# Kernel optimization log

Hardware: AMD Instinct MI355X
Metric: run time of the kernel (lower is better)

Reference implementation:

```python
import jax, jax.numpy as jnp
import numpy as np

N_NODES = 100000
N_EDGES = 1600000
N_GRAPHS = 256
D = 128
L = 3
N_OUT = 10


def setup_inputs() -> dict:
    key = jax.random.key(0)
    ks = jax.random.split(key, 6)
    x = jax.random.normal(ks[0], (N_NODES, D), dtype=jnp.float32)
    edge_index = jax.random.randint(ks[1], (2, N_EDGES), 0, N_NODES, dtype=jnp.int64)
    batch = jnp.sort(jax.random.randint(ks[2], (N_NODES,), 0, N_GRAPHS, dtype=jnp.int64))
    conv_w = jax.random.normal(ks[3], (L, D, D), dtype=jnp.float32) * (1.0 / np.sqrt(D))
    conv_b = jnp.zeros((L, D), dtype=jnp.float32)
    out_w = jax.random.normal(ks[4], (3 * D, N_OUT), dtype=jnp.float32) * (1.0 / np.sqrt(3 * D))
    out_b = jnp.zeros((N_OUT,), dtype=jnp.float32)
    return {"x": x, "edge_index": edge_index, "batch": batch,
            "conv_w": conv_w, "conv_b": conv_b, "out_w": out_w, "out_b": out_b}


def reference(x, edge_index, batch, conv_w, conv_b, out_w, out_b):
    N = x.shape[0]
    # --- add self-loops (PyG GCNConv default) ---
    loop = jnp.arange(N, dtype=edge_index.dtype)
    src = jnp.concatenate([edge_index[0], loop])  # [E+N]
    dst = jnp.concatenate([edge_index[1], loop])
    # --- symmetric normalization: deg computed on dst (col) ---
    deg = jax.ops.segment_sum(jnp.ones_like(dst, dtype=x.dtype), dst, num_segments=N)
    dinv = jnp.where(deg > 0, jax.lax.rsqrt(jnp.maximum(deg, 1.0)), 0.0)
    norm = dinv[src] * dinv[dst]  # [E+N]

    h = x
    for l in range(conv_w.shape[0]):
        h = h @ conv_w[l]                                   # [N, D] transform first
        msg = h[src] * norm[:, None]                        # gather + scale
        h = jax.ops.segment_sum(msg, dst, num_segments=N)   # scatter-add
        h = jax.nn.relu(h + conv_b[l])

    # --- global max / mean / add pooling over graphs ---
    B = N_GRAPHS
    gmax = jax.ops.segment_max(h, batch, num_segments=B)
    gsum = jax.ops.segment_sum(h, batch, num_segments=B)
    cnt = jax.ops.segment_sum(jnp.ones((N, 1), h.dtype), batch, num_segments=B)
    gmean = gsum / jnp.maximum(cnt, 1.0)
    pooled = jnp.concatenate([gmax, gmean, gsum], axis=1)   # [B, 3D]
    # dropout p=0.5 is identity in eval mode
    return pooled @ out_w + out_b
```

## Files before the change

kernel.cpp:

```cpp
#include <hip/hip_runtime.h>
#include <hip/hip_bf16.h>

#define D 128
#define NP 8
#define DPB 64
#define KPB (DPB * NP)
#define SUB 64
#define CAP_SUB 64

typedef __attribute__((ext_vector_type(8))) __bf16 bf16x8;
typedef __attribute__((ext_vector_type(4))) float f32x4;
typedef __attribute__((ext_vector_type(4))) short s16x4;
typedef __attribute__((ext_vector_type(8))) short s16x8;

static __device__ __forceinline__ short f2bf(float f) {
    union { float f; unsigned u; } in; in.f = f;
    unsigned u = in.u;
    u += 0x7fffu + ((u >> 16) & 1u);
    return (short)(u >> 16);
}

__global__ void k_bucket(const int* __restrict__ src, const int* __restrict__ dst,
                         int* __restrict__ bcnt, int* __restrict__ staging,
                         int E, int KBE) {
    int i = blockIdx.x * 256 + threadIdx.x;
    if (i >= E) return;
    int d = dst[i], s = src[i];
    int b = d >> 6;
    int key = ((d & 63) << 3) | (s >> 14);
    int j = blockIdx.x & (SUB - 1);
    int slot = atomicAdd(&bcnt[j * KBE + b], 1);
    if (slot < CAP_SUB) staging[((size_t)j * KBE + b) * CAP_SUB + slot] = (key << 17) | s;
}

__global__ void k_btot(const int* __restrict__ bcnt, int* __restrict__ btot, int KBE) {
    int b = blockIdx.x * 256 + threadIdx.x;
    if (b >= KBE) return;
    int v = 0;
    #pragma unroll
    for (int j = 0; j < SUB; j++) {
        int c = bcnt[j * KBE + b];
        v += (c > CAP_SUB) ? CAP_SUB : c;
    }
    btot[b] = v;
}

__global__ void k_bscan(const int* __restrict__ btot, int* __restrict__ bbase,
                        int* __restrict__ row_ptr, int nkeys, int KBE) {
    __shared__ int sm[512];
    __shared__ int carry;
    int t = threadIdx.x;
    if (t == 0) carry = 0;
    __syncthreads();
    for (int c0 = 0; c0 < KBE; c0 += 512) {
        int b = c0 + t;
        int v = (b < KBE) ? btot[b] : 0;
        sm[t] = v;
        __syncthreads();
        for (int off = 1; off < 512; off <<= 1) {
            int x = (t >= off) ? sm[t - off] : 0;
            __syncthreads();
            sm[t] += x;
            __syncthreads();
        }
        if (b < KBE) bbase[b] = sm[t] - v + carry;
        __syncthreads();
        if (t == 0) carry += sm[511];
        __syncthreads();
    }
    if (t == 0) { bbase[KBE] = carry; row_ptr[nkeys] = carry; }
}

__global__ __launch_bounds__(256) void k_build(
    const int* __restrict__ staging, const int* __restrict__ bcnt,
    const int* __restrict__ bbase, int* __restrict__ row_ptr,
    int* __restrict__ csr_src, float* __restrict__ dinv, int N, int KBE)
{
    const int b = blockIdx.x;
    const int tid = threadIdx.x;
    __shared__ int cnt[KPB];
    __shared__ int subn[SUB];
    __shared__ int chunkbuf[256];
    __shared__ int carry;

    if (tid < SUB) {
        int c = bcnt[tid * KBE + b];
        subn[tid] = (c > CAP_SUB) ? CAP_SUB : c;
    }
    for (int k = tid; k < KPB; k += 256) cnt[k] = 0;
    if (tid == 0) carry = 0;
    __syncthreads();

    const int base = bbase[b];
    const int nb = bbase[b + 1] - base;
    const int j = tid >> 2, l4 = tid & 3;
    const int* __restrict__ sreg = staging + ((size_t)j * KBE + b) * CAP_SUB;
    const int sn = subn[j];

    for (int e = l4; e < sn; e += 4)
        atomicAdd(&cnt[sreg[e] >> 17], 1);
    __syncthreads();

    #pragma unroll 1
    for (int c = 0; c < KPB / 256; c++) {
        int idx = c * 256 + tid;
        int v = cnt[idx];
        chunkbuf[tid] = v;
        __syncthreads();
        for (int off = 1; off < 256; off <<= 1) {
            int x = (tid >= off) ? chunkbuf[tid - off] : 0;
            __syncthreads();
            chunkbuf[tid] += x;
            __syncthreads();
        }
        cnt[idx] = chunkbuf[tid] - v + carry;
        __syncthreads();
        if (tid == 255) carry += chunkbuf[255];
        __syncthreads();
    }

    for (int k = tid; k < KPB; k += 256)
        row_ptr[(size_t)b * KPB + k] = base + cnt[k];
    for (int dl = tid; dl < DPB; dl += 256) {
        int d = b * DPB + dl;
        if (d < N) {
            int hi2 = (dl == DPB - 1) ? nb : cnt[(dl + 1) * NP];
            int deg = hi2 - cnt[dl * NP];
            dinv[d] = rsqrtf((float)deg + 1.0f);
        }
    }
    __syncthreads();

    for (int e = l4; e < sn; e += 4) {
        int w = sreg[e];
        int slot = base + atomicAdd(&cnt[w >> 17], 1);
        csr_src[slot] = w & 0x1FFFF;
    }
}

__global__ void k_gseg(const int* __restrict__ batch, int* __restrict__ gstart,
                       int* __restrict__ gcnt, int N, int B) {
    int g = blockIdx.x * blockDim.x + threadIdx.x;
    if (g > B) return;
    int lo = 0, hi = N;
    while (lo < hi) {
        int mid = (lo + hi) >> 1;
        if (batch[mid] < g) lo = mid + 1; else hi = mid;
    }
    gstart[g] = lo;
    if (g < B) {
        int lo2 = lo, hi2 = N;
        while (lo2 < hi2) {
            int mid = (lo2 + hi2) >> 1;
            if (batch[mid] < g + 1) lo2 = mid + 1; else hi2 = mid;
        }
        gcnt[g] = lo2 - lo;
    }
}

__global__ void k_cvt_x(const float* __restrict__ x, const float* __restrict__ dinv,
                        short* __restrict__ xb, int total4) {
    int i = blockIdx.x * blockDim.x + threadIdx.x;
    if (i < total4) {
        float d = dinv[i >> 5];
        float4 v = ((const float4*)x)[i];
        s16x4 o;
        o.x = f2bf(v.x * d); o.y = f2bf(v.y * d);
        o.z = f2bf(v.z * d); o.w = f2bf(v.w * d);
        ((s16x4*)xb)[i] = o;
    }
}

__global__ void k_cvt_w(const float* __restrict__ W, short* __restrict__ Wt, int total) {
    int i = blockIdx.x * blockDim.x + threadIdx.x;
    if (i < total) {
        int l = i >> 14;
        int rem = i & 16383;
        int n = rem >> 7;
        int k = rem & 127;
        Wt[i] = f2bf(W[(l << 14) + (k << 7) + n]);
    }
}

__global__ __launch_bounds__(256) void k_layer(
    const short* __restrict__ hin, const int* __restrict__ row_ptr,
    const int* __restrict__ csr_src, const float* __restrict__ dinv,
    const short* __restrict__ Wt, const float* __restrict__ bias,
    short* __restrict__ hout, float* __restrict__ hrelu, int N, int mode)
{
    __shared__ __align__(16) short tile[16 * 128];
    const int tid = threadIdx.x;
    const int wave = tid >> 6;
    const int lane = tid & 63;
    const int group = lane >> 4;
    const int lg = lane & 15;
    const int off = lg * 8;
    const int node_base = blockIdx.x * 16;
    const int r = wave * 4 + group;
    const int i = node_base + r;

    short* dstp = &tile[r * 128 + ((lg ^ (r & 7)) << 3)];
    if (i < N) {
        float acc[8];
        bf16x8 v = *(const bf16x8*)(hin + (size_t)i * D + off);
        #pragma unroll
        for (int k = 0; k < 8; k++) acc[k] = (float)v[k];

        int t = row_ptr[i * NP];
        const int end = row_ptr[i * NP + NP];
        for (; t + 4 <= end; t += 4) {
            int i0 = csr_src[t + 0], i1 = csr_src[t + 1];
            int i2 = csr_src[t + 2], i3 = csr_src[t + 3];
            bf16x8 v0 = *(const bf16x8*)(hin + (size_t)i0 * D + off);
            bf16x8 v1 = *(const bf16x8*)(hin + (size_t)i1 * D + off);
            bf16x8 v2 = *(const bf16x8*)(hin + (size_t)i2 * D + off);
            bf16x8 v3 = *(const bf16x8*)(hin + (size_t)i3 * D + off);
            #pragma unroll
            for (int k = 0; k < 8; k++)
                acc[k] += (((float)v0[k] + (float)v1[k]) + ((float)v2[k] + (float)v3[k]));
        }
        for (; t < end; t++) {
            int i0 = csr_src[t];
            bf16x8 v0 = *(const bf16x8*)(hin + (size_t)i0 * D + off);
            #pragma unroll
            for (int k = 0; k < 8; k++) acc[k] += (float)v0[k];
        }

        const float di = dinv[i];
        s16x8 o;
        #pragma unroll
        for (int k = 0; k < 8; k++) o[k] = f2bf(acc[k] * di);
        *(s16x8*)dstp = o;
    } else {
        s16x8 z = {0, 0, 0, 0, 0, 0, 0, 0};
        *(s16x8*)dstp = z;
    }
    __syncthreads();

    bf16x8 afrag[4];
    #pragma unroll
    for (int kt = 0; kt < 4; kt++)
        afrag[kt] = *(const bf16x8*)(&tile[lg * 128 + (((group + 4 * kt) ^ (lg & 7)) << 3)]);

    f32x4 acc2[2];
    #pragma unroll
    for (int nt = 0; nt < 2; nt++) { f32x4 z = {0.f, 0.f, 0.f, 0.f}; acc2[nt] = z; }
    #pragma unroll
    for (int nt = 0; nt < 2; nt++) {
        const short* bp = Wt + (size_t)(wave * 32 + nt * 16 + lg) * D + group * 8;
        #pragma unroll
        for (int kt = 0; kt < 4; kt++) {
            bf16x8 b = *(const bf16x8*)(bp + kt * 32);
            acc2[nt] = __builtin_amdgcn_mfma_f32_16x16x32_bf16(afrag[kt], b, acc2[nt], 0, 0, 0);
        }
    }

    float bcol[2];
    #pragma unroll
    for (int nt = 0; nt < 2; nt++) bcol[nt] = bias[wave * 32 + nt * 16 + lg];
    const int row0 = node_base + group * 4;
    #pragma unroll
    for (int i2 = 0; i2 < 4; i2++) {
        int r2 = row0 + i2;
        if (r2 < N) {
            if (mode == 0) {
                float dr = dinv[r2];
                #pragma unroll
                for (int nt = 0; nt < 2; nt++) {
                    int col = wave * 32 + nt * 16 + lg;
                    float val = fmaxf(acc2[nt][i2] + bcol[nt], 0.0f);
                    hout[(size_t)r2 * D + col] = f2bf(val * dr);
                }
            } else {
                #pragma unroll
                for (int nt = 0; nt < 2; nt++) {
                    int col = wave * 32 + nt * 16 + lg;
                    hrelu[(size_t)r2 * D + col] = fmaxf(acc2[nt][i2] + bcol[nt], 0.0f);
                }
            }
        }
    }
}

__global__ __launch_bounds__(256) void k_pool(const float* __restrict__ hrelu,
                                              const int* __restrict__ gstart,
                                              const int* __restrict__ gcnt,
                                              float* __restrict__ pmax,
                                              float* __restrict__ psum, int B) {
    int g = blockIdx.x >> 2;
    int q = blockIdx.x & 3;
    int c = threadIdx.x & 127;
    int p = threadIdx.x >> 7;
    int start = gstart[g];
    int endr = start + gcnt[g];

    float mx0 = 0.f, mx1 = 0.f, sm0 = 0.f, sm1 = 0.f;
    int r = start + q * 2 + p;
    for (; r + 8 < endr; r += 16) {
        float v0 = hrelu[(size_t)r * D + c];
        float v1 = hrelu[(size_t)(r + 8) * D + c];
        mx0 = fmaxf(mx0, v0); sm0 += v0;
        mx1 = fmaxf(mx1, v1); sm1 += v1;
    }
    if (r < endr) {
        float v0 = hrelu[(size_t)r * D + c];
        mx0 = fmaxf(mx0, v0); sm0 += v0;
    }
    float mx = fmaxf(mx0, mx1), sm = sm0 + sm1;

    __shared__ float smx[128], ssm[128];
    if (p == 1) { smx[c] = mx; ssm[c] = sm; }
    __syncthreads();
    if (p == 0) {
        pmax[((size_t)q * B + g) * D + c] = fmaxf(mx, smx[c]);
        psum[((size_t)q * B + g) * D + c] = sm + ssm[c];
    }
}

__global__ void k_final(const float* __restrict__ pmax, const float* __restrict__ psum,
                        const int* __restrict__ gcnt, const float* __restrict__ ow,
                        const float* __restrict__ ob, float* __restrict__ out, int B) {
    int g = blockIdx.x;
    int t = threadIdx.x;
    float part[10];
    #pragma unroll
    for (int o = 0; o < 10; o++) part[o] = 0.f;
    float invc = 1.0f / fmaxf((float)gcnt[g], 1.0f);
    for (int k = t; k < 3 * D; k += 64) {
        int c = (k < D) ? k : ((k < 2 * D) ? k - D : k - 2 * D);
        float pk;
        if (k < D) {
            float m = pmax[(size_t)g * D + c];
            #pragma unroll
            for (int q = 1; q < 4; q++) m = fmaxf(m, pmax[((size_t)q * B + g) * D + c]);
            pk = m;
        } else {
            float s = psum[(size_t)g * D + c];
            #pragma unroll
            for (int q = 1; q < 4; q++) s += psum[((size_t)q * B + g) * D + c];
            pk = (k < 2 * D) ? s * invc : s;
        }
        const float* w = ow + k * 10;
        #pragma unroll
        for (int o = 0; o < 10; o++) part[o] += pk * w[o];
    }
    #pragma unroll
    for (int off = 32; off > 0; off >>= 1)
        #pragma unroll
        for (int o = 0; o < 10; o++) part[o] += __shfl_down(part[o], off, 64);
    if (t == 0)
        #pragma unroll
        for (int o = 0; o < 10; o++) out[g * 10 + o] = part[o] + ob[o];
}

extern "C" void kernel_launch(void* const* d_in, const int* in_sizes, int n_in,
                              void* d_out, int out_size, void* d_ws, size_t ws_size,
                              hipStream_t stream) {
    const float* x     = (const float*)d_in[0];
    const int*   ei    = (const int*)d_in[1];
    const int*   batch = (const int*)d_in[2];
    const float* convw = (const float*)d_in[3];
    const float* convb = (const float*)d_in[4];
    const float* outw  = (const float*)d_in[5];
    const float* outb  = (const float*)d_in[6];
    float* out = (float*)d_out;

    const int N = in_sizes[0] / D;
    const int E = in_sizes[1] / 2;
    const int L = in_sizes[3] / (D * D);
    const int B = out_size / 10;

    const int* src = ei;
    const int* dst = ei + E;

    const int KBE   = (N + DPB - 1) / DPB;
    const int nkeys = KBE * KPB;

    char* p = (char*)d_ws;
    auto alloc = [&](size_t bytes) { char* r = p; p += (bytes + 255) & ~255ull; return r; };
    short* hb0     = (short*)alloc((size_t)N * D * 2);
    short* hb1     = (short*)alloc((size_t)N * D * 2);
    float* hrelu   = (float*)alloc((size_t)N * D * 4);
    short* Wt      = (short*)alloc((size_t)L * D * D * 2);
    int*   row_ptr = (int*)alloc(((size_t)nkeys + 1) * 4);
    int*   csr_src = (int*)alloc((size_t)E * 4);
    int*   bcnt    = (int*)alloc((size_t)SUB * KBE * 4);
    int*   btot    = (int*)alloc((size_t)KBE * 4);
    int*   bbase   = (int*)alloc(((size_t)KBE + 1) * 4);
    float* dinv    = (float*)alloc((size_t)N * 4);
    float* pmax    = (float*)alloc((size_t)4 * B * D * 4);
    float* psum    = (float*)alloc((size_t)4 * B * D * 4);
    int*   gcnt    = (int*)alloc((size_t)B * 4);
    int*   gstart  = (int*)alloc(((size_t)B + 1) * 4);

    int* staging = (int*)hrelu;

    hipMemsetAsync(bcnt, 0, (size_t)SUB * KBE * 4, stream);

    k_bucket<<<(E + 255) / 256, 256, 0, stream>>>(src, dst, bcnt, staging, E, KBE);
    k_gseg<<<1, 512, 0, stream>>>(batch, gstart, gcnt, N, B);
    k_btot<<<(KBE + 255) / 256, 256, 0, stream>>>(bcnt, btot, KBE);
    k_bscan<<<1, 512, 0, stream>>>(btot, bbase, row_ptr, nkeys, KBE);
    k_build<<<KBE, 256, 0, stream>>>(staging, bcnt, bbase, row_ptr, csr_src, dinv, N, KBE);
    k_cvt_x<<<((N * D / 4) + 255) / 256, 256, 0, stream>>>(x, dinv, hb0, N * D / 4);
    k_cvt_w<<<((L * D * D) + 255) / 256, 256, 0, stream>>>(convw, Wt, L * D * D);

    const int lblocks = (N + 15) / 16;
    k_layer<<<lblocks, 256, 0, stream>>>(hb0, row_ptr, csr_src, dinv, Wt,
                                         convb, hb1, hrelu, N, 0);
    k_layer<<<lblocks, 256, 0, stream>>>(hb1, row_ptr, csr_src, dinv, Wt + D * D,
                                         convb + D, hb0, hrelu, N, 0);
    k_layer<<<lblocks, 256, 0, stream>>>(hb0, row_ptr, csr_src, dinv, Wt + 2 * D * D,
                                         convb + 2 * D, hb1, hrelu, N, 1);

    k_pool<<<B * 4, 256, 0, stream>>>(hrelu, gstart, gcnt, pmax, psum, B);
    k_final<<<B, 64, 0, stream>>>(pmax, psum, gcnt, outw, outb, out, B);
}
```

Measured before the change: 454.7 us.

## Replace bucket prefix-scan with atomic cursor and cut kernel launches

Removes the k_btot and k_bscan kernels. Each k_build block now reserves its CSR segment with an atomicAdd on a global cursor and writes a per-block row_ptr that carries its own end sentinel, so k_layer indexes row_ptr with a per-block offset. It also folds graph-segment lookup into k_pool/k_final via binary search and merges the x and W conversion kernels into one launch. The aim is fewer launches and serial single-block scans; the cost is that CSR segments are laid out in nondeterministic block order, plus redundant binary searches.

```diff
diff --git a/kernel.cpp b/kernel.cpp
--- a/kernel.cpp
+++ b/kernel.cpp
@@ -18,6 +18,12 @@
     unsigned u = in.u;
     u += 0x7fffu + ((u >> 16) & 1u);
     return (short)(u >> 16);
+}
+
+static __device__ __forceinline__ int lower_bound(const int* __restrict__ a, int n, int v) {
+    int lo = 0, hi = n;
+    while (lo < hi) { int mid = (lo + hi) >> 1; if (a[mid] < v) lo = mid + 1; else hi = mid; }
+    return lo;
 }
 
 __global__ void k_bucket(const int* __restrict__ src, const int* __restrict__ dst,
@@ -33,47 +39,9 @@
     if (slot < CAP_SUB) staging[((size_t)j * KBE + b) * CAP_SUB + slot] = (key << 17) | s;
 }
 
-__global__ void k_btot(const int* __restrict__ bcnt, int* __restrict__ btot, int KBE) {
-    int b = blockIdx.x * 256 + threadIdx.x;
-    if (b >= KBE) return;
-    int v = 0;
-    #pragma unroll
-    for (int j = 0; j < SUB; j++) {
-        int c = bcnt[j * KBE + b];
-        v += (c > CAP_SUB) ? CAP_SUB : c;
-    }
-    btot[b] = v;
-}
-
-__global__ void k_bscan(const int* __restrict__ btot, int* __restrict__ bbase,
-                        int* __restrict__ row_ptr, int nkeys, int KBE) {
-    __shared__ int sm[512];
-    __shared__ int carry;
-    int t = threadIdx.x;
-    if (t == 0) carry = 0;
-    __syncthreads();
-    for (int c0 = 0; c0 < KBE; c0 += 512) {
-        int b = c0 + t;
-        int v = (b < KBE) ? btot[b] : 0;
-        sm[t] = v;
-        __syncthreads();
-        for (int off = 1; off < 512; off <<= 1) {
-            int x = (t >= off) ? sm[t - off] : 0;
-            __syncthreads();
-            sm[t] += x;
-            __syncthreads();
-        }
-        if (b < KBE) bbase[b] = sm[t] - v + carry;
-        __syncthreads();
-        if (t == 0) carry += sm[511];
-        __syncthreads();
-    }
-    if (t == 0) { bbase[KBE] = carry; row_ptr[nkeys] = carry; }
-}
-
 __global__ __launch_bounds__(256) void k_build(
     const int* __restrict__ staging, const int* __restrict__ bcnt,
-    const int* __restrict__ bbase, int* __restrict__ row_ptr,
+    int* __restrict__ cursor, int* __restrict__ row_ptr,
     int* __restrict__ csr_src, float* __restrict__ dinv, int N, int KBE)
 {
     const int b = blockIdx.x;
@@ -82,6 +50,7 @@
     __shared__ int subn[SUB];
     __shared__ int chunkbuf[256];
     __shared__ int carry;
+    __shared__ int sbase, snb;
 
     if (tid < SUB) {
         int c = bcnt[tid * KBE + b];
@@ -91,8 +60,14 @@
     if (tid == 0) carry = 0;
     __syncthreads();
 
-    const int base = bbase[b];
-    const int nb = bbase[b + 1] - base;
+    if (tid == 0) {
+        int nb = 0;
+        #pragma unroll
+        for (int j2 = 0; j2 < SUB; j2++) nb += subn[j2];
+        snb = nb;
+        sbase = atomicAdd(cursor, nb);
+    }
+
     const int j = tid >> 2, l4 = tid & 3;
     const int* __restrict__ sreg = staging + ((size_t)j * KBE + b) * CAP_SUB;
     const int sn = subn[j];
@@ -100,6 +75,8 @@
     for (int e = l4; e < sn; e += 4)
         atomicAdd(&cnt[sreg[e] >> 17], 1);
     __syncthreads();
+    const int base = sbase;
+    const int nb = snb;
 
     #pragma unroll 1
     for (int c = 0; c < KPB / 256; c++) {
@@ -119,8 +96,10 @@
         __syncthreads();
     }
 
+    const size_t rb = (size_t)b * (KPB + 1);
     for (int k = tid; k < KPB; k += 256)
-        row_ptr[(size_t)b * KPB + k] = base + cnt[k];
+        row_ptr[rb + k] = base + cnt[k];
+    if (tid == 0) row_ptr[rb + KPB] = base + nb;
     for (int dl = tid; dl < DPB; dl += 256) {
         int d = b * DPB + dl;
         if (d < N) {
@@ -138,29 +117,10 @@
     }
 }
 
-__global__ void k_gseg(const int* __restrict__ batch, int* __restrict__ gstart,
-                       int* __restrict__ gcnt, int N, int B) {
-    int g = blockIdx.x * blockDim.x + threadIdx.x;
-    if (g > B) return;
-    int lo = 0, hi = N;
-    while (lo < hi) {
-        int mid = (lo + hi) >> 1;
-        if (batch[mid] < g) lo = mid + 1; else hi = mid;
-    }
-    gstart[g] = lo;
-    if (g < B) {
-        int lo2 = lo, hi2 = N;
-        while (lo2 < hi2) {
-            int mid = (lo2 + hi2) >> 1;
-            if (batch[mid] < g + 1) lo2 = mid + 1; else hi2 = mid;
-        }
-        gcnt[g] = lo2 - lo;
-    }
-}
-
-__global__ void k_cvt_x(const float* __restrict__ x, const float* __restrict__ dinv,
-                        short* __restrict__ xb, int total4) {
-    int i = blockIdx.x * blockDim.x + threadIdx.x;
+__global__ void k_cvt(const float* __restrict__ x, const float* __restrict__ dinv,
+                      short* __restrict__ xb, const float* __restrict__ W,
+                      short* __restrict__ Wt, int total4, int totalw) {
+    int i = blockIdx.x * 256 + threadIdx.x;
     if (i < total4) {
         float d = dinv[i >> 5];
         float4 v = ((const float4*)x)[i];
@@ -168,17 +128,15 @@
         o.x = f2bf(v.x * d); o.y = f2bf(v.y * d);
         o.z = f2bf(v.z * d); o.w = f2bf(v.w * d);
         ((s16x4*)xb)[i] = o;
-    }
-}
-
-__global__ void k_cvt_w(const float* __restrict__ W, short* __restrict__ Wt, int total) {
-    int i = blockIdx.x * blockDim.x + threadIdx.x;
-    if (i < total) {
-        int l = i >> 14;
-        int rem = i & 16383;
-        int n = rem >> 7;
-        int k = rem & 127;
-        Wt[i] = f2bf(W[(l << 14) + (k << 7) + n]);
+    } else {
+        int w = i - total4;
+        if (w < totalw) {
+            int l = w >> 14;
+            int rem = w & 16383;
+            int n = rem >> 7;
+            int k = rem & 127;
+            Wt[w] = f2bf(W[(l << 14) + (k << 7) + n]);
+        }
     }
 }
 
@@ -206,8 +164,9 @@
         #pragma unroll
         for (int k = 0; k < 8; k++) acc[k] = (float)v[k];
 
-        int t = row_ptr[i * NP];
-        const int end = row_ptr[i * NP + NP];
+        const int rpb = i * NP + (i >> 6);
+        int t = row_ptr[rpb];
+        const int end = row_ptr[rpb + NP];
         for (; t + 4 <= end; t += 4) {
             int i0 = csr_src[t + 0], i1 = csr_src[t + 1];
             int i2 = csr_src[t + 2], i3 = csr_src[t + 3];
@@ -283,16 +242,20 @@
 }
 
 __global__ __launch_bounds__(256) void k_pool(const float* __restrict__ hrelu,
-                                              const int* __restrict__ gstart,
-                                              const int* __restrict__ gcnt,
+                                              const int* __restrict__ batch,
                                               float* __restrict__ pmax,
-                                              float* __restrict__ psum, int B) {
+                                              float* __restrict__ psum, int N, int B) {
     int g = blockIdx.x >> 2;
     int q = blockIdx.x & 3;
     int c = threadIdx.x & 127;
     int p = threadIdx.x >> 7;
-    int start = gstart[g];
-    int endr = start + gcnt[g];
+    __shared__ int ss, se;
+    if (threadIdx.x == 0) {
+        ss = lower_bound(batch, N, g);
+        se = lower_bound(batch, N, g + 1);
+    }
+    __syncthreads();
+    int start = ss, endr = se;
 
     float mx0 = 0.f, mx1 = 0.f, sm0 = 0.f, sm1 = 0.f;
     int r = start + q * 2 + p;
@@ -318,14 +281,18 @@
 }
 
 __global__ void k_final(const float* __restrict__ pmax, const float* __restrict__ psum,
-                        const int* __restrict__ gcnt, const float* __restrict__ ow,
-                        const float* __restrict__ ob, float* __restrict__ out, int B) {
+                        const int* __restrict__ batch, const float* __restrict__ ow,
+                        const float* __restrict__ ob, float* __restrict__ out,
+                        int N, int B) {
     int g = blockIdx.x;
     int t = threadIdx.x;
+    __shared__ int scnt;
+    if (t == 0) scnt = lower_bound(batch, N, g + 1) - lower_bound(batch, N, g);
+    __syncthreads();
     float part[10];
     #pragma unroll
     for (int o = 0; o < 10; o++) part[o] = 0.f;
-    float invc = 1.0f / fmaxf((float)gcnt[g], 1.0f);
+    float invc = 1.0f / fmaxf((float)scnt, 1.0f);
     for (int k = t; k < 3 * D; k += 64) {
         int c = (k < D) ? k : ((k < 2 * D) ? k - D : k - 2 * D);
         float pk;
@@ -373,8 +340,7 @@
     const int* src = ei;
     const int* dst = ei + E;
 
-    const int KBE   = (N + DPB - 1) / DPB;
-    const int nkeys = KBE * KPB;
+    const int KBE = (N + DPB - 1) / DPB;
 
     char* p = (char*)d_ws;
     auto alloc = [&](size_t bytes) { char* r = p; p += (bytes + 255) & ~255ull; return r; };
@@ -382,28 +348,23 @@
     short* hb1     = (short*)alloc((size_t)N * D * 2);
     float* hrelu   = (float*)alloc((size_t)N * D * 4);
     short* Wt      = (short*)alloc((size_t)L * D * D * 2);
-    int*   row_ptr = (int*)alloc(((size_t)nkeys + 1) * 4);
+    int*   row_ptr = (int*)alloc((size_t)KBE * (KPB + 1) * 4);
     int*   csr_src = (int*)alloc((size_t)E * 4);
-    int*   bcnt    = (int*)alloc((size_t)SUB * KBE * 4);
-    int*   btot    = (int*)alloc((size_t)KBE * 4);
-    int*   bbase   = (int*)alloc(((size_t)KBE + 1) * 4);
+    int*   bcnt    = (int*)alloc(((size_t)SUB * KBE + 1) * 4);
     float* dinv    = (float*)alloc((size_t)N * 4);
     float* pmax    = (float*)alloc((size_t)4 * B * D * 4);
     float* psum    = (float*)alloc((size_t)4 * B * D * 4);
-    int*   gcnt    = (int*)alloc((size_t)B * 4);
-    int*   gstart  = (int*)alloc(((size_t)B + 1) * 4);
-
+
+    int* cursor = bcnt + (size_t)SUB * KBE;
     int* staging = (int*)hrelu;
 
-    hipMemsetAsync(bcnt, 0, (size_t)SUB * KBE * 4, stream);
+    hipMemsetAsync(bcnt, 0, ((size_t)SUB * KBE + 1) * 4, stream);
 
     k_bucket<<<(E + 255) / 256, 256, 0, stream>>>(src, dst, bcnt, staging, E, KBE);
-    k_gseg<<<1, 512, 0, stream>>>(batch, gstart, gcnt, N, B);
-    k_btot<<<(KBE + 255) / 256, 256, 0, stream>>>(bcnt, btot, KBE);
-    k_bscan<<<1, 512, 0, stream>>>(btot, bbase, row_ptr, nkeys, KBE);
-    k_build<<<KBE, 256, 0, stream>>>(staging, bcnt, bbase, row_ptr, csr_src, dinv, N, KBE);
-    k_cvt_x<<<((N * D / 4) + 255) / 256, 256, 0, stream>>>(x, dinv, hb0, N * D / 4);
-    k_cvt_w<<<((L * D * D) + 255) / 256, 256, 0, stream>>>(convw, Wt, L * D * D);
+    k_build<<<KBE, 256, 0, stream>>>(staging, bcnt, cursor, row_ptr, csr_src, dinv, N, KBE);
+    const int total4 = N * D / 4, totalw = L * D * D;
+    k_cvt<<<(total4 + totalw + 255) / 256, 256, 0, stream>>>(x, dinv, hb0, convw, Wt,
+                                                             total4, totalw);
 
     const int lblocks = (N + 15) / 16;
     k_layer<<<lblocks, 256, 0, stream>>>(hb0, row_ptr, csr_src, dinv, Wt,
@@ -413,6 +374,6 @@
     k_layer<<<lblocks, 256, 0, stream>>>(hb0, row_ptr, csr_src, dinv, Wt + 2 * D * D,
                                          convb + 2 * D, hb1, hrelu, N, 1);
 
-    k_pool<<<B * 4, 256, 0, stream>>>(hrelu, gstart, gcnt, pmax, psum, B);
-    k_final<<<B, 64, 0, stream>>>(pmax, psum, gcnt, outw, outb, out, B);
-}
+    k_pool<<<B * 4, 256, 0, stream>>>(hrelu, batch, pmax, psum, N, B);
+    k_final<<<B, 64, 0, stream>>>(pmax, psum, batch, outw, outb, out, N, B);
+}
```

Measured after the change: 464.1 us. +2.1%, slower.
